# Optimization experiments

Hardware: AMD Instinct MI355X
Metric: run time of the kernel (lower is better)

## Reference

```python
import jax, jax.numpy as jnp
import numpy as np

N, E, D_IN, H, C, E_DIM, FF = 50000, 800000, 128, 8, 16, 16, 512
HC = H * C
LAMBDA_INIT = 0.8
NEG = 0.2
EPS = 1e-5


def setup_inputs() -> dict:
    key = jax.random.key(0)
    ks = jax.random.split(key, 24)
    n = lambda k, s, sc=1.0: jax.random.normal(k, s, dtype=jnp.float32) * sc
    return {
        "x": n(ks[0], (N, D_IN)),
        "edge_attr": n(ks[1], (E, E_DIM)),
        "W_l1": n(ks[2], (D_IN, HC), 0.05),
        "W_l2": n(ks[3], (D_IN, HC), 0.05),
        "att_l1": n(ks[4], (1, H, C), 0.1),
        "att_r1": n(ks[5], (1, H, C), 0.1),
        "att_l2": n(ks[6], (1, H, C), 0.1),
        "att_r2": n(ks[7], (1, H, C), 0.1),
        "W_e1": n(ks[8], (E_DIM, HC), 0.1),
        "att_e1": n(ks[9], (1, H, C), 0.1),
        "W_e2": n(ks[10], (E_DIM, HC), 0.1),
        "att_e2": n(ks[11], (1, H, C), 0.1),
        "lq1": n(ks[12], (H, C), 0.1),
        "lk1": n(ks[13], (H, C), 0.1),
        "lq2": n(ks[14], (H, C), 0.1),
        "lk2": n(ks[15], (H, C), 0.1),
        "rms_attn": jnp.ones((HC,), jnp.float32),
        "W_out": n(ks[16], (HC, HC), 0.05),
        "b_out": jnp.zeros((HC,), jnp.float32),
        "bias_extra": jnp.zeros((HC,), jnp.float32),
        "rms_layer": jnp.ones((HC,), jnp.float32),
        "W_ff1": n(ks[17], (HC, FF), 0.05),
        "b_ff1": jnp.zeros((FF,), jnp.float32),
        "W_ff2": n(ks[18], (FF, HC), 0.05),
        "b_ff2": jnp.zeros((HC,), jnp.float32),
        "edge_index": jax.random.randint(ks[19], (2, E), 0, N, dtype=jnp.int32),
    }


def _rmsnorm(x, scale):
    norm = jnp.sqrt(jnp.mean(x * x, axis=-1, keepdims=True) + EPS)
    return x / norm * scale


def _forward(x, edge_attr, W_l1, W_l2, att_l1, att_r1, att_l2, att_r2,
             W_e1, att_e1, W_e2, att_e2, lq1, lk1, lq2, lk2,
             rms_attn, W_out, b_out, bias_extra, rms_layer,
             W_ff1, b_ff1, W_ff2, b_ff2, edge_index):
    src0, dst0 = edge_index[0], edge_index[1]
    # add_self_loops(fill_value='mean'): self-loop edge_attr = mean of incoming edge attrs
    deg = jax.ops.segment_sum(jnp.ones((E,), x.dtype), dst0, num_segments=N)
    loop_attr = jax.ops.segment_sum(edge_attr, dst0, num_segments=N) / jnp.maximum(deg, 1.0)[:, None]
    ar = jnp.arange(N, dtype=src0.dtype)
    src = jnp.concatenate([src0, ar])
    dst = jnp.concatenate([dst0, ar])
    ea = jnp.concatenate([edge_attr, loop_attr], axis=0)  # [E+N, edge_dim]

    def attn_pass(xh, att_l, att_r, W_e, att_e):
        e = (ea @ W_e).reshape(-1, H, C)          # [E2, H, C]
        xi = xh[dst]                               # target features [E2,H,C]
        xj = xh[src]                               # source features [E2,H,C]
        alpha = (xi * att_l).sum(-1) + (xj * att_r).sum(-1) + (e * att_e).sum(-1)  # [E2,H]
        alpha = jnp.where(alpha >= 0, alpha, NEG * alpha)  # leaky_relu
        amax = jax.ops.segment_max(alpha, dst, num_segments=N)
        alpha = jnp.exp(alpha - amax[dst])
        denom = jax.ops.segment_sum(alpha, dst, num_segments=N)
        alpha = alpha / denom[dst]
        return jax.ops.segment_sum((xj + e) * alpha[..., None], dst, num_segments=N)  # [N,H,C]

    x1 = (x @ W_l1).reshape(N, H, C)
    x2 = (x @ W_l2).reshape(N, H, C)
    out1 = attn_pass(x1, att_l1, att_r1, W_e1, att_e1)
    out2 = attn_pass(x2, att_l2, att_r2, W_e2, att_e2)

    lam = jnp.exp((lq1 * lk1).sum(-1)) - jnp.exp((lq2 * lk2).sum(-1)) + LAMBDA_INIT  # [H]
    out = (out1 - lam[None, :, None] * out2).reshape(N, HC)
    out = _rmsnorm(out, rms_attn) * (1.0 - LAMBDA_INIT)
    out = out @ W_out + b_out + bias_extra

    # transformer layer: residual + pre-norm FFN
    h = x + out
    hn = _rmsnorm(h, rms_layer)
    ff = jax.nn.gelu(hn @ W_ff1 + b_ff1, approximate=False) @ W_ff2 + b_ff2
    return h + ff


def reference(x, edge_attr, W_l1, W_l2, att_l1, att_r1, att_l2, att_r2,
              W_e1, att_e1, W_e2, att_e2, lq1, lk1, lq2, lk2,
              rms_attn, W_out, b_out, bias_extra, rms_layer,
              W_ff1, b_ff1, W_ff2, b_ff2, edge_index):
    return _forward(x, edge_attr, W_l1, W_l2, att_l1, att_r1, att_l2, att_r2,
                    W_e1, att_e1, W_e2, att_e2, lq1, lk1, lq2, lk2,
                    rms_attn, W_out, b_out, bias_extra, rms_layer,
                    W_ff1, b_ff1, W_ff2, b_ff2, edge_index)
```

## Files before the change

### kernel.cpp

```cpp
#include <hip/hip_runtime.h>
#include <math.h>

constexpr int N_  = 50000;
constexpr int E_  = 800000;
constexpr int H_  = 8;
constexpr int C_  = 16;
constexpr int HC_ = 128;
constexpr int ED_ = 16;
constexpr int FF_ = 512;
constexpr int NT_ = 3125;
constexpr float NEG_ = 0.2f;
constexpr float EPS_ = 1e-5f;
constexpr float LAMBDA_INIT_ = 0.8f;
constexpr float LOG2E_ = 1.4426950408889634f;

typedef __attribute__((ext_vector_type(8))) short bf16x8;
typedef __attribute__((ext_vector_type(4))) float f32x4;
typedef __fp16 half2v __attribute__((ext_vector_type(2)));

__device__ __forceinline__ float gelu_exact(float v) {
    return 0.5f * v * (1.0f + erff(v * 0.70710678118654752440f));
}
__device__ __forceinline__ ushort f2bf(float f) {
    uint u = __float_as_uint(f);
    return (ushort)((u + 0x7FFFu + ((u >> 16) & 1u)) >> 16);
}
__device__ __forceinline__ ushort f2h(float f) {
    __fp16 h = (__fp16)f;
    return *(ushort*)&h;
}
__device__ __forceinline__ uint pkh2(float a, float b) {
    half2v h = __builtin_amdgcn_cvt_pkrtz(a, b);
    return *(uint*)&h;
}
__device__ __forceinline__ void uph2(uint u, float& a, float& b) {
    half2v h = *(half2v*)&u;
    a = (float)h.x; b = (float)h.y;
}

constexpr int WL12_ = 288 * 128;
constexpr int WO_   = 128 * 128;
constexpr int WF1_  = 512 * 128;
constexpr int WF2_  = 128 * 512;
constexpr int CVT_TOTAL_ = WL12_ + WO_ + WF1_ + WF2_ + 128 + 8 + E_;

__device__ void wconv(const float* __restrict__ W, ushort* __restrict__ Wt, int t, int K, int N) {
    int col = t / K, k = t - col * K;
    Wt[t] = f2bf(W[(size_t)k * N + col]);
}
__device__ void wconv_h(const float* __restrict__ W, ushort* __restrict__ Wt, int t, int K, int N) {
    int col = t / K, k = t - col * K;
    Wt[t] = f2h(W[(size_t)k * N + col]);
}

__global__ __launch_bounds__(256) void k_cvt(
        const float* __restrict__ Wl1, const float* __restrict__ al1w, const float* __restrict__ ar1w,
        const float* __restrict__ Wl2, const float* __restrict__ al2w, const float* __restrict__ ar2w,
        const float* __restrict__ Wout, const float* __restrict__ Wff1, const float* __restrict__ Wff2,
        const float* __restrict__ We1, const float* __restrict__ ae1,
        const float* __restrict__ We2, const float* __restrict__ ae2,
        const float* __restrict__ lq1, const float* __restrict__ lk1,
        const float* __restrict__ lq2, const float* __restrict__ lk2,
        const int* __restrict__ dst0,
        ushort* __restrict__ wl12t,
        ushort* __restrict__ woutt, ushort* __restrict__ wff1t, ushort* __restrict__ wff2t,
        float2* __restrict__ wc, float* __restrict__ lam,
        int* __restrict__ deg, int* __restrict__ rank) {
    int g = blockIdx.x * blockDim.x + threadIdx.x;
    if (g < WL12_) {
        int col = g >> 7, k = g & 127;
        const float* W = (col < 144) ? Wl1 : Wl2;
        const float* alw = (col < 144) ? al1w : al2w;
        const float* arw = (col < 144) ? ar1w : ar2w;
        int c = (col < 144) ? col : col - 144;
        float v;
        if (c < 128) {
            v = W[(size_t)k * HC_ + c];
        } else if (c < 136) {
            int h = c - 128; v = 0.f;
#pragma unroll
            for (int cc = 0; cc < 16; ++cc) v = fmaf(W[(size_t)k * HC_ + h * 16 + cc], alw[h * 16 + cc], v);
        } else {
            int h = c - 136; v = 0.f;
#pragma unroll
            for (int cc = 0; cc < 16; ++cc) v = fmaf(W[(size_t)k * HC_ + h * 16 + cc], arw[h * 16 + cc], v);
        }
        wl12t[g] = f2bf(v);
        return;
    }
    g -= WL12_;
    if (g < WO_) { wconv(Wout, woutt, g, 128, 128); return; }
    g -= WO_;
    if (g < WF1_) { wconv(Wff1, wff1t, g, 128, 512); return; }
    g -= WF1_;
    if (g < WF2_) { wconv_h(Wff2, wff2t, g, 512, 128); return; }
    g -= WF2_;
    if (g < 128) {
        int k = g >> 3, h = g & 7;
        float s1 = 0.f, s2 = 0.f;
#pragma unroll
        for (int c = 0; c < 16; ++c) {
            s1 = fmaf(We1[k * HC_ + h * 16 + c], ae1[h * 16 + c], s1);
            s2 = fmaf(We2[k * HC_ + h * 16 + c], ae2[h * 16 + c], s2);
        }
        wc[g] = make_float2(s1, s2);
        return;
    }
    g -= 128;
    if (g < 8) {
        float d1 = 0.f, d2 = 0.f;
#pragma unroll
        for (int k = 0; k < 16; ++k) {
            d1 = fmaf(lq1[g * 16 + k], lk1[g * 16 + k], d1);
            d2 = fmaf(lq2[g * 16 + k], lk2[g * 16 + k], d2);
        }
        lam[g] = __expf(d1) - __expf(d2) + LAMBDA_INIT_;
        return;
    }
    g -= 8;
    if (g < E_) {
        rank[g] = atomicAdd(&deg[dst0[g]], 1);
    }
}

__global__ __launch_bounds__(1024) void k_scan(const int* __restrict__ deg,
                                               int* __restrict__ offs) {
    __shared__ int part[1024];
    int t = threadIdx.x;
    const int CH = (N_ + 1023) / 1024;
    int b = t * CH;
    int e = min(N_, b + CH);
    int sum = 0;
    for (int i = b; i < e; ++i) sum += deg[i];
    part[t] = sum;
    __syncthreads();
    for (int off = 1; off < 1024; off <<= 1) {
        int v = (t >= off) ? part[t - off] : 0;
        __syncthreads();
        part[t] += v;
        __syncthreads();
    }
    int run = (t == 0) ? 0 : part[t - 1];
    for (int i = b; i < e; ++i) {
        offs[i] = run;
        run += deg[i];
    }
    if (t == 1023) offs[N_] = run;
}

__global__ __launch_bounds__(256) void k_fill(const int* __restrict__ src0,
                                              const int* __restrict__ dst0,
                                              const int* __restrict__ offs,
                                              const int* __restrict__ rank,
                                              int* __restrict__ csr_src,
                                              int2* __restrict__ csr_de) {
    int e = blockIdx.x * blockDim.x + threadIdx.x;
    if (e >= E_) return;
    int d = dst0[e];
    int p = offs[d] + rank[e];
    csr_src[p] = src0[e];
    csr_de[p] = make_int2(d, e);
}

__global__ __launch_bounds__(256) void k_et(const float* __restrict__ eattr,
                                            const float2* __restrict__ all_,
                                            const float2* __restrict__ arr_,
                                            const float2* __restrict__ wc,
                                            const int* __restrict__ csr_src,
                                            const int2* __restrict__ csr_de,
                                            uint* __restrict__ rec) {
    __shared__ float2 wcs[128];
    int t = threadIdx.x;
    if (t < 128) wcs[t] = wc[t];
    __syncthreads();
    int p = blockIdx.x * blockDim.x + t;
    if (p >= E_) return;
    int2 de = csr_de[p];
    int dst = de.x, eid = de.y;
    int src = csr_src[p];
    const float* ea = eattr + (size_t)eid * ED_;
    float eav[16];
    {
        float4 q0 = *(const float4*)(ea + 0);
        float4 q1 = *(const float4*)(ea + 4);
        float4 q2 = *(const float4*)(ea + 8);
        float4 q3 = *(const float4*)(ea + 12);
        eav[0] = q0.x; eav[1] = q0.y; eav[2] = q0.z; eav[3] = q0.w;
        eav[4] = q1.x; eav[5] = q1.y; eav[6] = q1.z; eav[7] = q1.w;
        eav[8] = q2.x; eav[9] = q2.y; eav[10] = q2.z; eav[11] = q2.w;
        eav[12] = q3.x; eav[13] = q3.y; eav[14] = q3.z; eav[15] = q3.w;
    }
    const float2* alp = all_ + (size_t)dst * 8;
    const float2* arp = arr_ + (size_t)src * 8;
    uint ra[8], re[8];
#pragma unroll
    for (int h = 0; h < 8; ++h) {
        float t1 = 0.f, t2 = 0.f;
#pragma unroll
        for (int k = 0; k < 16; ++k) {
            float2 w = wcs[k * 8 + h];
            t1 = fmaf(eav[k], w.x, t1);
            t2 = fmaf(eav[k], w.y, t2);
        }
        float2 al = alp[h], ar = arp[h];
        float a1 = al.x + ar.x + t1;
        a1 = ((a1 >= 0.f) ? a1 : NEG_ * a1) * LOG2E_;
        float a2 = al.y + ar.y + t2;
        a2 = ((a2 >= 0.f) ? a2 : NEG_ * a2) * LOG2E_;
        ra[h] = pkh2(exp2f(a1), exp2f(a2));
    }
#pragma unroll
    for (int i = 0; i < 8; ++i) re[i] = pkh2(eav[2 * i], eav[2 * i + 1]);
    uint4* rp = (uint4*)(rec + (size_t)p * 16);
    rp[0] = make_uint4(ra[0], ra[1], ra[2], ra[3]);
    rp[1] = make_uint4(ra[4], ra[5], ra[6], ra[7]);
    rp[2] = make_uint4(re[0], re[1], re[2], re[3]);
    rp[3] = make_uint4(re[4], re[5], re[6], re[7]);
}

__global__ __launch_bounds__(256) void k_agg(const ushort* __restrict__ x12,
                                             const float2* __restrict__ all_,
                                             const float2* __restrict__ arr_,
                                             const uint* __restrict__ rec,
                                             const float2* __restrict__ wcg,
                                             const float* __restrict__ We1, const float* __restrict__ We2,
                                             const float* __restrict__ lam, const float* __restrict__ rms_attn,
                                             const int* __restrict__ offs, const int* __restrict__ csr_src,
                                             ushort* __restrict__ attn_out) {
    int wid = (int)((blockIdx.x * blockDim.x + threadIdx.x) >> 6);
    if (wid >= N_) return;
    int lane = threadIdx.x & 63;
    int h = lane >> 3;
    int cp = lane & 7;
    int e0 = h * C_ + cp * 2;
    int hbase = lane & 56;

    int s = offs[wid], eend = offs[wid + 1];
    int deg = eend - s;

    float s1 = 0.f, s2 = 0.f;
    float ax1x = 0.f, ax1y = 0.f, ax2x = 0.f, ax2y = 0.f;
    float ws1x = 0.f, ws1y = 0.f, ws2x = 0.f, ws2y = 0.f;
    float esx = 0.f, esy = 0.f;

    auto accum = [&](uint ua, uint ue, uint2 ux) {
        float p1, p2, eax, eay, x1a, x2a, x1b, x2b;
        uph2(ua, p1, p2);
        uph2(ue, eax, eay);
        uph2(ux.x, x1a, x2a);
        uph2(ux.y, x1b, x2b);
        s1 += p1; s2 += p2;
        ax1x = fmaf(p1, x1a, ax1x); ax1y = fmaf(p1, x1b, ax1y);
        ax2x = fmaf(p2, x2a, ax2x); ax2y = fmaf(p2, x2b, ax2y);
        ws1x = fmaf(p1, eax, ws1x); ws1y = fmaf(p1, eay, ws1y);
        ws2x = fmaf(p2, eax, ws2x); ws2y = fmaf(p2, eay, ws2y);
        esx += eax; esy += eay;
    };

    int j = s;
    for (; j + 3 < eend; j += 4) {
        int srcv[4];
#pragma unroll
        for (int q = 0; q < 4; ++q) srcv[q] = csr_src[j + q];
        uint uav[4], uev[4];
        uint2 uxv[4];
#pragma unroll
        for (int q = 0; q < 4; ++q) {
            const uint* r = rec + (size_t)(j + q) * 16;
            uav[q] = r[h];
            uev[q] = r[8 + cp];
            uxv[q] = *(const uint2*)(x12 + (size_t)srcv[q] * 256 + e0 * 2);
        }
#pragma unroll
        for (int q = 0; q < 4; ++q) accum(uav[q], uev[q], uxv[q]);
    }
    for (; j < eend; ++j) {
        int src = csr_src[j];
        const uint* r = rec + (size_t)j * 16;
        uint ua = r[h];
        uint ue = r[8 + cp];
        uint2 ux = *(const uint2*)(x12 + (size_t)src * 256 + e0 * 2);
        accum(ua, ue, ux);
    }

    float invdeg = 1.0f / (float)max(deg, 1);
    float esmx = esx * invdeg, esmy = esy * invdeg;

    float2 w0 = wcg[(2 * cp) * 8 + h];
    float2 w1 = wcg[(2 * cp + 1) * 8 + h];
    float tp1 = esmx * w0.x + esmy * w1.x;
    float tp2 = esmx * w0.y + esmy * w1.y;
    tp1 += __shfl_xor(tp1, 1); tp1 += __shfl_xor(tp1, 2); tp1 += __shfl_xor(tp1, 4);
    tp2 += __shfl_xor(tp2, 1); tp2 += __shfl_xor(tp2, 2); tp2 += __shfl_xor(tp2, 4);

    float2 alv = all_[(size_t)wid * 8 + h];
    float2 arv = arr_[(size_t)wid * 8 + h];
    float aS1 = alv.x + arv.x + tp1;
    aS1 = ((aS1 >= 0.f) ? aS1 : NEG_ * aS1) * LOG2E_;
    float aS2 = alv.y + arv.y + tp2;
    aS2 = ((aS2 >= 0.f) ? aS2 : NEG_ * aS2) * LOG2E_;
    float pS1 = exp2f(aS1), pS2 = exp2f(aS2);
    {
        uint2 ux = *(const uint2*)(x12 + (size_t)wid * 256 + e0 * 2);
        float x1a, x2a, x1b, x2b;
        uph2(ux.x, x1a, x2a);
        uph2(ux.y, x1b, x2b);
        s1 += pS1; s2 += pS2;
        ax1x = fmaf(pS1, x1a, ax1x); ax1y = fmaf(pS1, x1b, ax1y);
        ax2x = fmaf(pS2, x2a, ax2x); ax2y = fmaf(pS2, x2b, ax2y);
        ws1x = fmaf(pS1, esmx, ws1x); ws1y = fmaf(pS1, esmy, ws1y);
        ws2x = fmaf(pS2, esmx, ws2x); ws2y = fmaf(pS2, esmy, ws2y);
    }

    float o1x = ax1x, o1y = ax1y, o2x = ax2x, o2y = ax2y;
#pragma unroll
    for (int kp = 0; kp < 8; ++kp) {
        float wa1 = __shfl(ws1x, hbase + kp), wb1 = __shfl(ws1y, hbase + kp);
        float wa2 = __shfl(ws2x, hbase + kp), wb2 = __shfl(ws2y, hbase + kp);
        float2 a0 = *(const float2*)(We1 + (2 * kp) * HC_ + e0);
        float2 a1 = *(const float2*)(We1 + (2 * kp + 1) * HC_ + e0);
        float2 b0 = *(const float2*)(We2 + (2 * kp) * HC_ + e0);
        float2 b1 = *(const float2*)(We2 + (2 * kp + 1) * HC_ + e0);
        o1x = fmaf(wa1, a0.x, o1x); o1x = fmaf(wb1, a1.x, o1x);
        o1y = fmaf(wa1, a0.y, o1y); o1y = fmaf(wb1, a1.y, o1y);
        o2x = fmaf(wa2, b0.x, o2x); o2x = fmaf(wb2, b1.x, o2x);
        o2y = fmaf(wa2, b0.y, o2y); o2y = fmaf(wb2, b1.y, o2y);
    }
    float inv1 = 1.0f / s1, inv2 = 1.0f / s2;
    o1x *= inv1; o1y *= inv1; o2x *= inv2; o2y *= inv2;

    float lamh = lam[h];
    float v0 = o1x - lamh * o2x;
    float v1 = o1y - lamh * o2y;

    float ss = v0 * v0 + v1 * v1;
#pragma unroll
    for (int mk = 1; mk < 64; mk <<= 1) ss += __shfl_xor(ss, mk);
    float rn = rsqrtf(ss * (1.0f / 128.0f) + EPS_);
    float g0 = rms_attn[e0] * (1.0f - LAMBDA_INIT_);
    float g1 = rms_attn[e0 + 1] * (1.0f - LAMBDA_INIT_);
    ushort2 o;
    o.x = f2bf(v0 * rn * g0);
    o.y = f2bf(v1 * rn * g1);
    *(ushort2*)(attn_out + (size_t)wid * HC_ + e0) = o;
}

__global__ __launch_bounds__(256) void k_g0(const float* __restrict__ x,
                                            const ushort* __restrict__ wl12t,
                                            ushort* __restrict__ x12,
                                            float* __restrict__ alr,
                                            float* __restrict__ arr) {
    int tid = threadIdx.x;
    int w = tid >> 6, lane = tid & 63;
    int lrow = lane & 15, kg = lane >> 4;
    int cg = w & 1, rh = w >> 1;

    bf16x8 B[9][4];
#pragma unroll
    for (int c = 0; c < 9; ++c) {
        int ct = cg * 9 + c;
#pragma unroll
        for (int ks = 0; ks < 4; ++ks)
            B[c][ks] = *(const bf16x8*)(wl12t + (size_t)(ct * 16 + lrow) * 128 + ks * 32 + kg * 8);
    }

    for (int tile = blockIdx.x * 2 + rh; tile < NT_; tile += gridDim.x * 2) {
        int r0 = tile * 16;
        const float* Ap = x + (size_t)(r0 + lrow) * 128 + kg * 8;
        bf16x8 af[4];
#pragma unroll
        for (int ks = 0; ks < 4; ++ks) {
            float4 qa = *(const float4*)(Ap + ks * 32);
            float4 qb = *(const float4*)(Ap + ks * 32 + 4);
            bf16x8 t;
            t[0] = (short)f2bf(qa.x); t[1] = (short)f2bf(qa.y);
            t[2] = (short)f2bf(qa.z); t[3] = (short)f2bf(qa.w);
            t[4] = (short)f2bf(qb.x); t[5] = (short)f2bf(qb.y);
            t[6] = (short)f2bf(qb.z); t[7] = (short)f2bf(qb.w);
            af[ks] = t;
        }
        f32x4 acc[9];
#pragma unroll
        for (int c = 0; c < 9; ++c) acc[c] = (f32x4){0.f, 0.f, 0.f, 0.f};
#pragma unroll
        for (int ks = 0; ks < 4; ++ks)
#pragma unroll
            for (int c = 0; c < 9; ++c)
                acc[c] = __builtin_amdgcn_mfma_f32_16x16x32_bf16(af[ks], B[c][ks], acc[c], 0, 0, 0);

#pragma unroll
        for (int c = 0; c < 8; ++c) {
            int col = c * 16 + lrow;
#pragma unroll
            for (int jj = 0; jj < 4; ++jj) {
                int r = r0 + kg * 4 + jj;
                x12[(size_t)r * 256 + col * 2 + cg] = f2h(acc[c][jj]);
            }
        }
#pragma unroll
        for (int jj = 0; jj < 4; ++jj) {
            int r = r0 + kg * 4 + jj;
            float v = acc[8][jj];
            if (lrow < 8) alr[((size_t)r * 8 + lrow) * 2 + cg] = v;
            else          arr[((size_t)r * 8 + (lrow - 8)) * 2 + cg] = v;
        }
    }
}

__global__ __launch_bounds__(256) void k_g1(const ushort* __restrict__ attn,
                                            const ushort* __restrict__ woutt,
                                            const float* __restrict__ b1,
                                            const float* __restrict__ b2,
                                            const float* __restrict__ res,
                                            const float* __restrict__ scale,
                                            float* __restrict__ hbuf,
                                            ushort* __restrict__ hn) {
    int tid = threadIdx.x;
    int w = tid >> 6, lane = tid & 63;
    int lrow = lane & 15, kg = lane >> 4;

    bf16x8 B[8][4];
#pragma unroll
    for (int c = 0; c < 8; ++c)
#pragma unroll
        for (int ks = 0; ks < 4; ++ks)
            B[c][ks] = *(const bf16x8*)(woutt + (size_t)(c * 16 + lrow) * 128 + ks * 32 + kg * 8);

    for (int tile = blockIdx.x * 4 + w; tile < NT_; tile += gridDim.x * 4) {
        int r0 = tile * 16;
        const ushort* Ap = attn + (size_t)(r0 + lrow) * 128 + kg * 8;
        bf16x8 af[4];
#pragma unroll
        for (int ks = 0; ks < 4; ++ks) af[ks] = *(const bf16x8*)(Ap + ks * 32);
        f32x4 acc[8];
#pragma unroll
        for (int c = 0; c < 8; ++c) acc[c] = (f32x4){0.f, 0.f, 0.f, 0.f};
#pragma unroll
        for (int ks = 0; ks < 4; ++ks)
#pragma unroll
            for (int c = 0; c < 8; ++c)
                acc[c] = __builtin_amdgcn_mfma_f32_16x16x32_bf16(af[ks], B[c][ks], acc[c], 0, 0, 0);

        float ssj[4] = {0.f, 0.f, 0.f, 0.f};
#pragma unroll
        for (int c = 0; c < 8; ++c) {
            int col = c * 16 + lrow;
            float bv = b1[col] + b2[col];
#pragma unroll
            for (int jj = 0; jj < 4; ++jj) {
                int r = r0 + kg * 4 + jj;
                float v = acc[c][jj] + bv + res[(size_t)r * HC_ + col];
                acc[c][jj] = v;
                ssj[jj] += v * v;
            }
        }
        float rn[4];
#pragma unroll
        for (int jj = 0; jj < 4; ++jj) {
            float ss = ssj[jj];
            ss += __shfl_xor(ss, 1); ss += __shfl_xor(ss, 2);
            ss += __shfl_xor(ss, 4); ss += __shfl_xor(ss, 8);
            rn[jj] = rsqrtf(ss * (1.0f / 128.0f) + EPS_);
        }
#pragma unroll
        for (int c = 0; c < 8; ++c) {
            int col = c * 16 + lrow;
            float sc = scale[col];
#pragma unroll
            for (int jj = 0; jj < 4; ++jj) {
                int r = r0 + kg * 4 + jj;
                float v = acc[c][jj];
                hbuf[(size_t)r * HC_ + col] = v;
                hn[(size_t)r * HC_ + col] = f2bf(v * rn[jj] * sc);
            }
        }
    }
}

__global__ __launch_bounds__(256) void k_ff1(const ushort* __restrict__ hn,
                                             const ushort* __restrict__ wff1t,
                                             const float* __restrict__ bff1,
                                             ushort* __restrict__ g) {
    int tid = threadIdx.x;
    int w = tid >> 6, lane = tid & 63;
    int lrow = lane & 15, kg = lane >> 4;

    bf16x8 B[8][4];
#pragma unroll
    for (int c = 0; c < 8; ++c)
#pragma unroll
        for (int ks = 0; ks < 4; ++ks)
            B[c][ks] = *(const bf16x8*)(wff1t + (size_t)(w * 128 + c * 16 + lrow) * 128 + ks * 32 + kg * 8);

    for (int tile = blockIdx.x; tile < NT_; tile += gridDim.x) {
        int r0 = tile * 16;
        const ushort* Ap = hn + (size_t)(r0 + lrow) * 128 + kg * 8;
        bf16x8 af[4];
#pragma unroll
        for (int ks = 0; ks < 4; ++ks) af[ks] = *(const bf16x8*)(Ap + ks * 32);
        f32x4 acc[8];
#pragma unroll
        for (int c = 0; c < 8; ++c) acc[c] = (f32x4){0.f, 0.f, 0.f, 0.f};
#pragma unroll
        for (int ks = 0; ks < 4; ++ks)
#pragma unroll
            for (int c = 0; c < 8; ++c)
                acc[c] = __builtin_amdgcn_mfma_f32_16x16x32_bf16(af[ks], B[c][ks], acc[c], 0, 0, 0);

#pragma unroll
        for (int c = 0; c < 8; ++c) {
            int col = w * 128 + c * 16 + lrow;
            float bv = bff1[col];
#pragma unroll
            for (int jj = 0; jj < 4; ++jj) {
                float v = gelu_exact(acc[c][jj] + bv);
                float other = __shfl_xor(v, 1);
                if (!(lrow & 1)) {
                    int r = r0 + kg * 4 + jj;
                    ((uint*)g)[(size_t)r * 256 + (col >> 1)] = pkh2(v, other);
                }
            }
        }
    }
}

__global__ __launch_bounds__(256) void k_ff2(const ushort* __restrict__ g,
                                             const ushort* __restrict__ wff2t,
                                             const float* __restrict__ bff2,
                                             const float* __restrict__ hres,
                                             float* __restrict__ out) {
    int tid = threadIdx.x;
    int w = tid >> 6, lane = tid & 63;
    int lrow = lane & 15, kg = lane >> 4;

    bf16x8 B[2][16];
#pragma unroll
    for (int c = 0; c < 2; ++c)
#pragma unroll
        for (int ks = 0; ks < 16; ++ks)
            B[c][ks] = *(const bf16x8*)(wff2t + (size_t)((2 * w + c) * 16 + lrow) * 512 + ks * 32 + kg * 8);

    for (int tile = blockIdx.x; tile < NT_; tile += gridDim.x) {
        int r0 = tile * 16;
        const ushort* Ap = g + (size_t)(r0 + lrow) * 512 + kg * 8;
        f32x4 acc[2];
        acc[0] = (f32x4){0.f, 0.f, 0.f, 0.f};
        acc[1] = (f32x4){0.f, 0.f, 0.f, 0.f};
#pragma unroll
        for (int ks = 0; ks < 16; ++ks) {
            bf16x8 af = *(const bf16x8*)(Ap + ks * 32);
            acc[0] = __builtin_amdgcn_mfma_f32_16x16x32_f16(af, B[0][ks], acc[0], 0, 0, 0);
            acc[1] = __builtin_amdgcn_mfma_f32_16x16x32_f16(af, B[1][ks], acc[1], 0, 0, 0);
        }
#pragma unroll
        for (int c = 0; c < 2; ++c) {
            int col = (2 * w + c) * 16 + lrow;
            float bv = bff2[col];
#pragma unroll
            for (int jj = 0; jj < 4; ++jj) {
                int r = r0 + kg * 4 + jj;
                out[(size_t)r * HC_ + col] = acc[c][jj] + bv + hres[(size_t)r * HC_ + col];
            }
        }
    }
}

extern "C" void kernel_launch(void* const* d_in, const int* in_sizes, int n_in,
                              void* d_out, int out_size, void* d_ws, size_t ws_size,
                              hipStream_t stream) {
    const float* x        = (const float*)d_in[0];
    const float* eattr    = (const float*)d_in[1];
    const float* W_l1     = (const float*)d_in[2];
    const float* W_l2     = (const float*)d_in[3];
    const float* att_l1   = (const float*)d_in[4];
    const float* att_r1   = (const float*)d_in[5];
    const float* att_l2   = (const float*)d_in[6];
    const float* att_r2   = (const float*)d_in[7];
    const float* W_e1     = (const float*)d_in[8];
    const float* att_e1   = (const float*)d_in[9];
    const float* W_e2     = (const float*)d_in[10];
    const float* att_e2   = (const float*)d_in[11];
    const float* lq1      = (const float*)d_in[12];
    const float* lk1      = (const float*)d_in[13];
    const float* lq2      = (const float*)d_in[14];
    const float* lk2      = (const float*)d_in[15];
    const float* rms_attn = (const float*)d_in[16];
    const float* W_out    = (const float*)d_in[17];
    const float* b_out    = (const float*)d_in[18];
    const float* bias_x   = (const float*)d_in[19];
    const float* rms_layer= (const float*)d_in[20];
    const float* W_ff1    = (const float*)d_in[21];
    const float* b_ff1    = (const float*)d_in[22];
    const float* W_ff2    = (const float*)d_in[23];
    const float* b_ff2    = (const float*)d_in[24];
    const int*   eidx     = (const int*)d_in[25];
    const int* src0 = eidx;
    const int* dst0 = eidx + E_;
    float* out = (float*)d_out;

    char* base = (char*)d_ws;
    size_t off = 0;
    auto alloc = [&](size_t bytes) -> char* {
        off = (off + 255) & ~(size_t)255;
        char* p = base + off;
        off += bytes;
        return p;
    };
    const size_t NF = (size_t)N_ * HC_;
    float*  f_h    = (float*)alloc(NF * 4);
    ushort* f_hnat = (ushort*)alloc(NF * 2);
    ushort* f_x12  = (ushort*)alloc(NF * 2 * 2);
    char*   f_rg   = alloc((size_t)E_ * 64);
    uint*   f_rec  = (uint*)f_rg;
    ushort* f_g    = (ushort*)f_rg;
    ushort* w_l12t = (ushort*)alloc((size_t)288 * 128 * 2);
    ushort* w_outt = (ushort*)alloc((size_t)HC_ * HC_ * 2);
    ushort* w_ff1t = (ushort*)alloc((size_t)HC_ * FF_ * 2);
    ushort* w_ff2t = (ushort*)alloc((size_t)FF_ * HC_ * 2);
    float2* f_all  = (float2*)alloc((size_t)N_ * H_ * 8);
    float2* f_arr  = (float2*)alloc((size_t)N_ * H_ * 8);
    float2* f_wc   = (float2*)alloc(128 * 8);
    float*  f_lam  = (float*)alloc(256);
    int*  i_deg  = (int*)alloc((size_t)N_ * 4);
    int*  i_offs = (int*)alloc((size_t)(N_ + 1) * 4);
    int*  i_rank = (int*)alloc((size_t)E_ * 4);
    int*  i_csr  = (int*)alloc((size_t)E_ * 4);
    int2* i_de   = (int2*)alloc((size_t)E_ * 8);
    (void)ws_size;

    hipMemsetAsync(i_deg, 0, (size_t)N_ * 4, stream);

    k_cvt<<<dim3((CVT_TOTAL_ + 255) / 256), dim3(256), 0, stream>>>(
        W_l1, att_l1, att_r1, W_l2, att_l2, att_r2, W_out, W_ff1, W_ff2,
        W_e1, att_e1, W_e2, att_e2, lq1, lk1, lq2, lk2, dst0,
        w_l12t, w_outt, w_ff1t, w_ff2t, f_wc, f_lam, i_deg, i_rank);

    k_scan<<<dim3(1), dim3(1024), 0, stream>>>(i_deg, i_offs);
    k_fill<<<dim3((E_ + 255) / 256), dim3(256), 0, stream>>>(src0, dst0, i_offs, i_rank,
                                                             i_csr, i_de);

    k_g0<<<dim3(512), dim3(256), 0, stream>>>(x, w_l12t, f_x12,
                                              (float*)f_all, (float*)f_arr);

    k_et<<<dim3(E_ / 256), dim3(256), 0, stream>>>(eattr, f_all, f_arr, f_wc,
                                                   i_csr, i_de, f_rec);

    k_agg<<<dim3((N_ + 3) / 4), dim3(256), 0, stream>>>(
        f_x12, f_all, f_arr, f_rec, f_wc,
        W_e1, W_e2, f_lam, rms_attn, i_offs, i_csr, f_hnat);

    k_g1<<<dim3(256), dim3(256), 0, stream>>>(f_hnat, w_outt, b_out, bias_x, x,
                                              rms_layer, f_h, f_hnat);

    k_ff1<<<dim3(512), dim3(256), 0, stream>>>(f_hnat, w_ff1t, b_ff1, f_g);
    k_ff2<<<dim3(1024), dim3(256), 0, stream>>>(f_g, w_ff2t, b_ff2, f_h, out);
}
```

Baseline: 441.6 us.

## Bucket nodes by degree for aggregation and unroll edge loop by eight with prefetch

Builds a degree histogram in the scan kernel and a new permutation kernel that groups destination nodes by in-degree. The aggregation kernel then processes nodes in that order so waves in a block see similar edge counts, reducing load imbalance. The inner edge loop is widened to eight edges per step, and the next batch of source indices is prefetched while the current batch accumulates. This adds a kernel launch and atomics, scatters the node order (hurting locality of output writes and offsets reads), and raises register pressure.

```diff
diff --git a/kernel.cpp b/kernel.cpp
--- a/kernel.cpp
+++ b/kernel.cpp
@@ -124,12 +124,15 @@
 }
 
 __global__ __launch_bounds__(1024) void k_scan(const int* __restrict__ deg,
-                                               int* __restrict__ offs) {
+                                               int* __restrict__ offs,
+                                               int* __restrict__ bktcur) {
     __shared__ int part[1024];
+    __shared__ int hist[64];
     int t = threadIdx.x;
     const int CH = (N_ + 1023) / 1024;
     int b = t * CH;
     int e = min(N_, b + CH);
+    if (t < 64) hist[t] = 0;
     int sum = 0;
     for (int i = b; i < e; ++i) sum += deg[i];
     part[t] = sum;
@@ -144,8 +147,27 @@
     for (int i = b; i < e; ++i) {
         offs[i] = run;
         run += deg[i];
+        atomicAdd(&hist[min(deg[i], 63)], 1);
     }
     if (t == 1023) offs[N_] = run;
+    __syncthreads();
+    if (t == 0) {
+        int r2 = 0;
+        for (int d = 0; d < 64; ++d) {
+            bktcur[d] = r2;
+            r2 += hist[d];
+        }
+    }
+}
+
+__global__ __launch_bounds__(256) void k_perm(const int* __restrict__ deg,
+                                              int* __restrict__ bktcur,
+                                              int* __restrict__ perm) {
+    int i = blockIdx.x * blockDim.x + threadIdx.x;
+    if (i >= N_) return;
+    int d = min(deg[i], 63);
+    int pos = atomicAdd(&bktcur[d], 1);
+    perm[pos] = i;
 }
 
 __global__ __launch_bounds__(256) void k_fill(const int* __restrict__ src0,
@@ -226,9 +248,11 @@
                                              const float* __restrict__ We1, const float* __restrict__ We2,
                                              const float* __restrict__ lam, const float* __restrict__ rms_attn,
                                              const int* __restrict__ offs, const int* __restrict__ csr_src,
+                                             const int* __restrict__ perm,
                                              ushort* __restrict__ attn_out) {
-    int wid = (int)((blockIdx.x * blockDim.x + threadIdx.x) >> 6);
-    if (wid >= N_) return;
+    int slot = (int)((blockIdx.x * blockDim.x + threadIdx.x) >> 6);
+    if (slot >= N_) return;
+    int wid = perm[slot];
     int lane = threadIdx.x & 63;
     int h = lane >> 3;
     int cp = lane & 7;
@@ -257,24 +281,34 @@
         esx += eax; esy += eay;
     };
 
-    int j = s;
-    for (; j + 3 < eend; j += 4) {
-        int srcv[4];
-#pragma unroll
-        for (int q = 0; q < 4; ++q) srcv[q] = csr_src[j + q];
-        uint uav[4], uev[4];
-        uint2 uxv[4];
-#pragma unroll
-        for (int q = 0; q < 4; ++q) {
-            const uint* r = rec + (size_t)(j + q) * 16;
+    int nb = deg >> 3;
+    int srcv[8];
+    if (nb > 0) {
+#pragma unroll
+        for (int q = 0; q < 8; ++q) srcv[q] = csr_src[s + q];
+    }
+    for (int b = 0; b < nb; ++b) {
+        int jb = s + b * 8;
+        uint uav[8], uev[8];
+        uint2 uxv[8];
+#pragma unroll
+        for (int q = 0; q < 8; ++q) {
+            const uint* r = rec + (size_t)(jb + q) * 16;
             uav[q] = r[h];
             uev[q] = r[8 + cp];
             uxv[q] = *(const uint2*)(x12 + (size_t)srcv[q] * 256 + e0 * 2);
         }
-#pragma unroll
-        for (int q = 0; q < 4; ++q) accum(uav[q], uev[q], uxv[q]);
-    }
-    for (; j < eend; ++j) {
+        int srcn[8];
+        if (b + 1 < nb) {
+#pragma unroll
+            for (int q = 0; q < 8; ++q) srcn[q] = csr_src[jb + 8 + q];
+        }
+#pragma unroll
+        for (int q = 0; q < 8; ++q) accum(uav[q], uev[q], uxv[q]);
+#pragma unroll
+        for (int q = 0; q < 8; ++q) srcv[q] = srcn[q];
+    }
+    for (int j = s + nb * 8; j < eend; ++j) {
         int src = csr_src[j];
         const uint* r = rec + (size_t)j * 16;
         uint ua = r[h];
@@ -626,6 +660,8 @@
     int*  i_rank = (int*)alloc((size_t)E_ * 4);
     int*  i_csr  = (int*)alloc((size_t)E_ * 4);
     int2* i_de   = (int2*)alloc((size_t)E_ * 8);
+    int*  i_perm = (int*)alloc((size_t)N_ * 4);
+    int*  i_bkt  = (int*)alloc(64 * 4);
     (void)ws_size;
 
     hipMemsetAsync(i_deg, 0, (size_t)N_ * 4, stream);
@@ -635,7 +671,8 @@
         W_e1, att_e1, W_e2, att_e2, lq1, lk1, lq2, lk2, dst0,
         w_l12t, w_outt, w_ff1t, w_ff2t, f_wc, f_lam, i_deg, i_rank);
 
-    k_scan<<<dim3(1), dim3(1024), 0, stream>>>(i_deg, i_offs);
+    k_scan<<<dim3(1), dim3(1024), 0, stream>>>(i_deg, i_offs, i_bkt);
+    k_perm<<<dim3((N_ + 255) / 256), dim3(256), 0, stream>>>(i_deg, i_bkt, i_perm);
     k_fill<<<dim3((E_ + 255) / 256), dim3(256), 0, stream>>>(src0, dst0, i_offs, i_rank,
                                                              i_csr, i_de);
 
@@ -647,7 +684,7 @@
 
     k_agg<<<dim3((N_ + 3) / 4), dim3(256), 0, stream>>>(
         f_x12, f_all, f_arr, f_rec, f_wc,
-        W_e1, W_e2, f_lam, rms_attn, i_offs, i_csr, f_hnat);
+        W_e1, W_e2, f_lam, rms_attn, i_offs, i_csr, i_perm, f_hnat);
 
     k_g1<<<dim3(256), dim3(256), 0, stream>>>(f_hnat, w_outt, b_out, bias_x, x,
                                               rms_layer, f_h, f_hnat);
```

Result: slower. 586.9 us (+32.9%).
